# Kernel tuning notes

Measured on AMD Instinct MI355X. Metric: run time of the kernel, lower is better.

The kernel has to match this reference:

```python
import jax, jax.numpy as jnp
import numpy as np

A = 128       # atom_fea_len
NBR = 41      # nbr_fea_len
H = 128       # h_fea_len_dist == h_fea_len_const
NCONV = 3
EPS = 1e-5    # BatchNorm eps


def leaky(x):
    return jnp.where(x >= 0, x, 0.01 * x)  # LeakyReLU(0.01)


def bn(x2d, g, b):
    # training-mode BatchNorm1d: batch statistics over dim 0 (biased variance)
    mu = x2d.mean(0)
    var = x2d.var(0)
    return g * (x2d - mu) * jax.lax.rsqrt(var + EPS) + b


def setup_inputs() -> dict:
    N, M = 20000, 12
    key = jax.random.key(0)
    ks = jax.random.split(key, 24)
    s = 0.02
    in2 = 2 * A + NBR  # 297
    d = {}
    d["atom_fea"] = jax.random.normal(ks[0], (N, 92), jnp.float32)
    d["nbr_fea"] = jax.random.uniform(ks[1], (N, M, NBR), dtype=jnp.float32)
    d["nbr_fea_offset"] = jax.random.normal(ks[2], (N, M, 3), jnp.float32)
    d["atom_pos"] = jax.random.normal(ks[3], (N, 3), jnp.float32) * 3.0
    d["cells"] = jnp.eye(3, dtype=jnp.float32) * 10.0 + 0.1 * jax.random.normal(ks[4], (3, 3), jnp.float32)
    d["nbr_fea_idx"] = jax.random.randint(ks[5], (N, M), 0, N)
    # embedding
    d["emb_W"] = s * jax.random.normal(ks[6], (A, 92), jnp.float32)
    d["emb_b"] = jnp.zeros((A,), jnp.float32)
    # conv layers (stacked)
    d["convs_W"] = s * jax.random.normal(ks[7], (NCONV, 2 * A, in2), jnp.float32)
    d["convs_b"] = jnp.zeros((NCONV, 2 * A), jnp.float32)
    d["convs_bn1_g"] = jnp.ones((NCONV, 2 * A), jnp.float32)
    d["convs_bn1_b"] = jnp.zeros((NCONV, 2 * A), jnp.float32)
    d["convs_bn2_g"] = jnp.ones((NCONV, A), jnp.float32)
    d["convs_bn2_b"] = jnp.zeros((NCONV, A), jnp.float32)
    # bond_distance head
    d["dist_W"] = s * jax.random.normal(ks[8], (H, in2), jnp.float32)
    d["dist_b"] = jnp.zeros((H,), jnp.float32)
    d["dist_bn_g"] = jnp.ones((H,), jnp.float32)
    d["dist_bn_b"] = jnp.zeros((H,), jnp.float32)
    d["dist2_W"] = s * jax.random.normal(ks[9], (1, H), jnp.float32)
    d["dist2_b"] = jnp.zeros((1,), jnp.float32)
    # bond_constant head
    d["const_W"] = s * jax.random.normal(ks[10], (H, in2), jnp.float32)
    d["const_b"] = jnp.zeros((H,), jnp.float32)
    d["const_bn_g"] = jnp.ones((H,), jnp.float32)
    d["const_bn_b"] = jnp.zeros((H,), jnp.float32)
    d["const2_W"] = s * jax.random.normal(ks[11], (1, H), jnp.float32)
    d["const2_b"] = jnp.zeros((1,), jnp.float32)
    return d


def _forward(atom_fea, nbr_fea, nbr_fea_offset, atom_pos, cells,
             emb_W, emb_b, convs_W, convs_b, convs_bn1_g, convs_bn1_b,
             convs_bn2_g, convs_bn2_b, dist_W, dist_b, dist_bn_g, dist_bn_b,
             dist2_W, dist2_b, const_W, const_b, const_bn_g, const_bn_b,
             const2_W, const2_b, nbr_fea_idx):
    N, M = nbr_fea_idx.shape
    af = atom_fea @ emb_W.T + emb_b  # (N, A) embedding

    # get_distance: PBC distance using fractional offsets and the cell matrix
    nbr_abs = atom_pos[nbr_fea_idx] + jnp.einsum('nmk,kd->nmd', nbr_fea_offset, cells)
    dvec = nbr_abs - atom_pos[:, None, :]
    distance = jnp.sqrt(jnp.sum(dvec * dvec, -1, keepdims=True) + 1e-12)  # (N, M, 1)

    # conv layers: gather -> concat -> linear -> bn -> gate -> sum -> bn -> residual
    for i in range(NCONV):
        total = jnp.concatenate([
            jnp.broadcast_to(af[:, None, :], (N, M, A)),
            af[nbr_fea_idx],
            nbr_fea], axis=2)                                   # (N, M, 2A+NBR)
        g = jnp.einsum('nmf,of->nmo', total, convs_W[i]) + convs_b[i]  # (N, M, 2A)
        g = bn(g.reshape(-1, 2 * A), convs_bn1_g[i], convs_bn1_b[i]).reshape(N, M, 2 * A)
        nbr_filter = jax.nn.sigmoid(g[..., :A])
        nbr_core = leaky(g[..., A:])
        summed = bn((nbr_filter * nbr_core).sum(1), convs_bn2_g[i], convs_bn2_b[i])
        af = leaky(af + summed)

    # bond features
    bond_fea = jnp.concatenate([
        jnp.broadcast_to(af[:, None, :], (N, M, A)),
        af[nbr_fea_idx],
        nbr_fea], axis=2)  # (N, M, 2A+NBR)

    # bond_distance head (LeakyReLU activations)
    bd = jnp.einsum('nmf,hf->nmh', bond_fea, dist_W) + dist_b
    bd = leaky(bn(bd.reshape(-1, H), dist_bn_g, dist_bn_b).reshape(N, M, H))
    bd = leaky(jnp.einsum('nmh,oh->nmo', bd, dist2_W) + dist2_b + distance)  # (N, M, 1)

    # bond_constant head (Softplus activations)
    bc = jnp.einsum('nmf,hf->nmh', bond_fea, const_W) + const_b
    bc = jax.nn.softplus(bn(bc.reshape(-1, H), const_bn_g, const_bn_b).reshape(N, M, H))
    bc = jax.nn.softplus(jnp.einsum('nmh,oh->nmo', bc, const2_W) + const2_b)  # (N, M, 1)

    return jnp.concatenate([bd, bc], axis=-1)  # (N, M, 2)


def reference(atom_fea, nbr_fea, nbr_fea_offset, atom_pos, cells,
              emb_W, emb_b, convs_W, convs_b, convs_bn1_g, convs_bn1_b,
              convs_bn2_g, convs_bn2_b, dist_W, dist_b, dist_bn_g, dist_bn_b,
              dist2_W, dist2_b, const_W, const_b, const_bn_g, const_bn_b,
              const2_W, const2_b, nbr_fea_idx):
    return _forward(atom_fea, nbr_fea, nbr_fea_offset, atom_pos, cells,
                    emb_W, emb_b, convs_W, convs_b, convs_bn1_g, convs_bn1_b,
                    convs_bn2_g, convs_bn2_b, dist_W, dist_b, dist_bn_g, dist_bn_b,
                    dist2_W, dist2_b, const_W, const_b, const_bn_g, const_bn_b,
                    const2_W, const2_b, nbr_fea_idx)
```

## Files before the change

### kernel.cpp

```cpp
#include <hip/hip_runtime.h>
#include <hip/hip_bf16.h>
#include <math.h>

typedef __hip_bfloat16 bf16;

#define AFEA 128
#define NBRF 41
#define IN2 297
#define KP 320
#define TSTR 328
#define ROWS 64
#define P1 64
#define P2 16

typedef __attribute__((ext_vector_type(8))) short bf16x8;
typedef __attribute__((ext_vector_type(4))) float f32x4;

__device__ __forceinline__ unsigned short bfbits(float x) {
    bf16 h = __float2bfloat16(x);
    return *(unsigned short*)&h;
}
__device__ __forceinline__ unsigned int pack2(float x, float y) {
    return (unsigned int)bfbits(x) | ((unsigned int)bfbits(y) << 16);
}
__device__ __forceinline__ float blo(unsigned int u) { return __uint_as_float(u << 16); }
__device__ __forceinline__ float bhi(unsigned int u) { return __uint_as_float(u & 0xffff0000u); }
__device__ __forceinline__ float leakyf(float x) { return x >= 0.f ? x : 0.01f * x; }
__device__ __forceinline__ float sigmoid_fast(float x) { return 1.f / (1.f + __expf(-x)); }
__device__ __forceinline__ float softplus_fast(float x) {
    return fmaxf(x, 0.f) + __logf(1.f + __expf(-fabsf(x)));
}

__global__ void nbr16_kernel(const float* __restrict__ nbr, unsigned short* __restrict__ nbr16,
                             int NM)
{
    int i = blockIdx.x * blockDim.x + threadIdx.x;
    if (i >= NM * 64) return;
    int k = i & 63, e = i >> 6;
    nbr16[i] = (k < NBRF) ? bfbits(nbr[(size_t)e * NBRF + k]) : 0;
}

__global__ __launch_bounds__(256) void embed_kernel(
    const float* __restrict__ xf, const float* __restrict__ W,
    const float* __restrict__ b, float* __restrict__ af,
    unsigned short* __restrict__ af16, int N)
{
    __shared__ float W_s[92 * 128];
    __shared__ float xs[16 * 92];
    int t = threadIdx.x;
    int n0 = blockIdx.x * 16;
    for (int i = t; i < 92 * 128; i += 256) {
        int o = i / 92, k = i - o * 92;
        W_s[k * 128 + o] = W[i];
    }
    for (int i = t; i < 16 * 92; i += 256) {
        int a = i / 92, k = i - a * 92;
        int n = n0 + a;
        xs[i] = (n < N) ? xf[(size_t)n * 92 + k] : 0.f;
    }
    __syncthreads();
    int o = t & 127, h = t >> 7;
    float bias = b[o];
    for (int a = h; a < 16; a += 2) {
        int n = n0 + a;
        if (n >= N) break;
        float acc = bias;
        const float* xr = xs + a * 92;
        #pragma unroll 4
        for (int k = 0; k < 92; k++) acc += xr[k] * W_s[k * 128 + o];
        af[(size_t)n * AFEA + o] = acc;
        af16[(size_t)n * AFEA + o] = bfbits(acc);
    }
}

__global__ void prep_kernel(const float* __restrict__ Wa, size_t offA,
                            const float* __restrict__ Wsrc, size_t offB,
                            unsigned short* __restrict__ Wb,
                            float* __restrict__ zbuf, int nz)
{
    int i = blockIdx.x * blockDim.x + threadIdx.x;
    if (i < nz) zbuf[i] = 0.f;
    if (i >= KP * 256) return;
    int t32 = i & 31;
    int c = (i >> 5) & 255;
    int kc = i >> 13;
    int k = kc * 32 + t32;
    float v = 0.f;
    if (k < IN2) v = (c < 128) ? Wa[offA + (size_t)c * IN2 + k]
                               : Wsrc[offB + (size_t)(c - 128) * IN2 + k];
    Wb[i] = bfbits(v);
}

__global__ __launch_bounds__(256, 3) void gemm_mfma_kernel(
    const unsigned short* __restrict__ af16, const unsigned short* __restrict__ nbr16,
    const int* __restrict__ idx, const unsigned short* __restrict__ Wb,
    const float* __restrict__ bias_a, size_t boffA,
    const float* __restrict__ bias_b, size_t boffB,
    unsigned short* __restrict__ g_t, float* __restrict__ part1,
    int NM, int M)
{
    __shared__ unsigned short a_tile[ROWS * TSTR];
    const int t = threadIdx.x;
    const int e0 = blockIdx.x * ROWS;

    const int l = t & 63, w = t >> 6;
    const int m16 = l & 15, q = l >> 4;
    const int colbase = w * 64;
    const unsigned short* bbase = Wb + (size_t)(colbase + m16) * 32 + q * 8;

    {
        int row = t >> 2, p = t & 3;
        int e = e0 + row;
        int n = e / M;
        int j = idx[e];
        const uint4* srcn = (const uint4*)(af16 + (size_t)n * AFEA);
        const uint4* srcj = (const uint4*)(af16 + (size_t)j * AFEA);
        const uint4* srcb = (const uint4*)(nbr16 + (size_t)e * 64);
        uint4* dst = (uint4*)(a_tile + row * TSTR);
        #pragma unroll
        for (int u = 0; u < 4; u++) dst[p + 4 * u] = srcn[p + 4 * u];
        #pragma unroll
        for (int u = 0; u < 4; u++) dst[16 + p + 4 * u] = srcj[p + 4 * u];
        #pragma unroll
        for (int u = 0; u < 2; u++) dst[32 + p + 4 * u] = srcb[p + 4 * u];
    }

    bf16x8 bcur[4], bnxt[4];
    #pragma unroll
    for (int ct = 0; ct < 4; ct++)
        bcur[ct] = *(const bf16x8*)(bbase + ct * 512);
    #pragma unroll
    for (int ct = 0; ct < 4; ct++)
        bnxt[ct] = *(const bf16x8*)(bbase + 8192 + ct * 512);

    __syncthreads();

    f32x4 acc[4][4];
    #pragma unroll
    for (int rt = 0; rt < 4; rt++)
        #pragma unroll
        for (int ct = 0; ct < 4; ct++) acc[rt][ct] = (f32x4)0.f;

    const unsigned short* abase = a_tile + m16 * TSTR + q * 8;

    #pragma unroll
    for (int kc = 0; kc < KP / 32; kc++) {
        bf16x8 a[4], b2[4];
        if (kc < KP / 32 - 2) {
            #pragma unroll
            for (int ct = 0; ct < 4; ct++)
                b2[ct] = *(const bf16x8*)(bbase + (kc + 2) * 8192 + ct * 512);
        }
        #pragma unroll
        for (int rt = 0; rt < 4; rt++)
            a[rt] = *(const bf16x8*)(abase + rt * 16 * TSTR + kc * 32);
        #pragma unroll
        for (int rt = 0; rt < 4; rt++)
            #pragma unroll
            for (int ct = 0; ct < 4; ct++)
                acc[rt][ct] = __builtin_amdgcn_mfma_f32_16x16x32_bf16(
                    a[rt], bcur[ct], acc[rt][ct], 0, 0, 0);
        if (kc < KP / 32 - 1) {
            #pragma unroll
            for (int ct = 0; ct < 4; ct++) bcur[ct] = bnxt[ct];
        }
        if (kc < KP / 32 - 2) {
            #pragma unroll
            for (int ct = 0; ct < 4; ct++) bnxt[ct] = b2[ct];
        }
    }

    float* pp = part1 + (size_t)(blockIdx.x & (P1 - 1)) * 512;
    #pragma unroll
    for (int ct = 0; ct < 4; ct++) {
        int col = colbase + ct * 16 + m16;
        float bias = (col < 128) ? bias_a[boffA + col] : bias_b[boffB + col - 128];
        float ps = 0.f, pq = 0.f;
        #pragma unroll
        for (int rt = 0; rt < 4; rt++) {
            float v0 = acc[rt][ct][0] + bias;
            float v1 = acc[rt][ct][1] + bias;
            float v2 = acc[rt][ct][2] + bias;
            float v3 = acc[rt][ct][3] + bias;
            ps += (v0 + v1) + (v2 + v3);
            pq += (v0 * v0 + v1 * v1) + (v2 * v2 + v3 * v3);
            uint2 pk;
            pk.x = pack2(v0, v1);
            pk.y = pack2(v2, v3);
            *(uint2*)(g_t + (size_t)col * NM + e0 + rt * 16 + q * 4) = pk;
        }
        ps += __shfl_xor(ps, 16); ps += __shfl_xor(ps, 32);
        pq += __shfl_xor(pq, 16); pq += __shfl_xor(pq, 32);
        if (q == 0) {
            atomicAdd(&pp[col], ps);
            atomicAdd(&pp[256 + col], pq);
        }
    }
}

__global__ __launch_bounds__(256) void gate_kernel(
    const unsigned short* __restrict__ gt, const float* __restrict__ part1,
    const float* __restrict__ gamma, const float* __restrict__ beta,
    float* __restrict__ summed, float* __restrict__ part2,
    float cnt1, int N, int M, int NM)
{
    __shared__ float affA[4 * 16], affC[4 * 16];
    int t = threadIdx.x, w = t >> 6, l = t & 63;
    int cp0 = (blockIdx.x & 3) * 16 + w * 4;
    int fch0 = 2 * cp0;

    if (l < 16) {
        int ch = (l < 8) ? (fch0 + l) : (128 + fch0 + (l - 8));
        float s = 0.f, qq = 0.f;
        #pragma unroll 8
        for (int p = 0; p < P1; p++) {
            s += part1[(size_t)p * 512 + ch];
            qq += part1[(size_t)p * 512 + 256 + ch];
        }
        float mean = s / cnt1;
        float var = fmaxf(qq / cnt1 - mean * mean, 0.f);
        float a = gamma[ch] * rsqrtf(var + 1e-5f);
        affA[w * 16 + l] = a;
        affC[w * 16 + l] = beta[ch] - mean * a;
    }
    __syncthreads();

    int n = (blockIdx.x >> 2) * 64 + l;
    bool act = (n < N);
    size_t col0 = (size_t)n * M;
    float* pp = part2 + (size_t)(blockIdx.x & (P2 - 1)) * 256;
    #pragma unroll
    for (int cpi = 0; cpi < 4; cpi++) {
        int chf = fch0 + 2 * cpi;
        int chc = 128 + chf;
        float s0 = 0.f, s1 = 0.f;
        if (act) {
            const uint2* rf0 = (const uint2*)(gt + (size_t)chf * NM + col0);
            const uint2* rf1 = (const uint2*)(gt + (size_t)(chf + 1) * NM + col0);
            const uint2* rc0 = (const uint2*)(gt + (size_t)chc * NM + col0);
            const uint2* rc1 = (const uint2*)(gt + (size_t)(chc + 1) * NM + col0);
            float aF0 = affA[w * 16 + 2 * cpi],     cF0 = affC[w * 16 + 2 * cpi];
            float aF1 = affA[w * 16 + 2 * cpi + 1], cF1 = affC[w * 16 + 2 * cpi + 1];
            float aC0 = affA[w * 16 + 8 + 2 * cpi],     cC0 = affC[w * 16 + 8 + 2 * cpi];
            float aC1 = affA[w * 16 + 8 + 2 * cpi + 1], cC1 = affC[w * 16 + 8 + 2 * cpi + 1];
            #pragma unroll
            for (int u = 0; u < 3; u++) {
                uint2 f0 = rf0[u], f1 = rf1[u], k0 = rc0[u], k1 = rc1[u];
                #pragma unroll
                for (int h = 0; h < 4; h++) {
                    unsigned int fw0 = (h < 2) ? f0.x : f0.y;
                    unsigned int fw1 = (h < 2) ? f1.x : f1.y;
                    unsigned int kw0 = (h < 2) ? k0.x : k0.y;
                    unsigned int kw1 = (h < 2) ? k1.x : k1.y;
                    float gf0 = (h & 1) ? bhi(fw0) : blo(fw0);
                    float gf1 = (h & 1) ? bhi(fw1) : blo(fw1);
                    float gc0 = (h & 1) ? bhi(kw0) : blo(kw0);
                    float gc1 = (h & 1) ? bhi(kw1) : blo(kw1);
                    s0 += sigmoid_fast(fmaf(aF0, gf0, cF0)) * leakyf(fmaf(aC0, gc0, cC0));
                    s1 += sigmoid_fast(fmaf(aF1, gf1, cF1)) * leakyf(fmaf(aC1, gc1, cC1));
                }
            }
            *(float2*)(summed + (size_t)n * AFEA + chf) = make_float2(s0, s1);
        }
        float q0 = s0 * s0, q1 = s1 * s1;
        #pragma unroll
        for (int sft = 32; sft > 0; sft >>= 1) {
            s0 += __shfl_xor(s0, sft);
            s1 += __shfl_xor(s1, sft);
            q0 += __shfl_xor(q0, sft);
            q1 += __shfl_xor(q1, sft);
        }
        if (l == 0) {
            atomicAdd(&pp[chf], s0);
            atomicAdd(&pp[chf + 1], s1);
            atomicAdd(&pp[128 + chf], q0);
            atomicAdd(&pp[128 + chf + 1], q1);
        }
    }
}

__global__ __launch_bounds__(256) void afup_kernel(
    float* __restrict__ af, unsigned short* __restrict__ af16,
    const float* __restrict__ summed, const float* __restrict__ part2,
    const float* __restrict__ gamma2, const float* __restrict__ beta2,
    float cnt2, int total)
{
    __shared__ float a2s[128], c2s[128];
    int t = threadIdx.x;
    if (t < 128) {
        float s = 0.f, qq = 0.f;
        #pragma unroll
        for (int p = 0; p < P2; p++) {
            s += part2[(size_t)p * 256 + t];
            qq += part2[(size_t)p * 256 + 128 + t];
        }
        float mean = s / cnt2;
        float var = fmaxf(qq / cnt2 - mean * mean, 0.f);
        float a = gamma2[t] * rsqrtf(var + 1e-5f);
        a2s[t] = a;
        c2s[t] = beta2[t] - mean * a;
    }
    __syncthreads();
    int o = t & 127;
    float a2 = a2s[o], c2 = c2s[o];
    int base = blockIdx.x * 2048 + t;
    #pragma unroll
    for (int k = 0; k < 8; k++) {
        int i = base + k * 256;
        if (i < total) {
            float v = af[i] + a2 * summed[i] + c2;
            v = (v >= 0.f) ? v : 0.01f * v;
            af[i] = v;
            af16[i] = bfbits(v);
        }
    }
}

__global__ __launch_bounds__(256) void head_kernel(
    const unsigned short* __restrict__ gt, const float* __restrict__ part1,
    const float* __restrict__ dbg, const float* __restrict__ cbg,
    const float* __restrict__ dbb, const float* __restrict__ cbb,
    const float* __restrict__ w2d, const float* __restrict__ b2d,
    const float* __restrict__ w2c, const float* __restrict__ b2c,
    const float* __restrict__ pos, const float* __restrict__ off,
    const float* __restrict__ cells, const int* __restrict__ idx,
    float* __restrict__ out, float cnt1, int NM, int M)
{
    __shared__ float a_s[256], c_s[256], w_s[256];
    int t = threadIdx.x;
    {
        float s = 0.f, qq = 0.f;
        #pragma unroll 8
        for (int p = 0; p < P1; p++) {
            s += part1[(size_t)p * 512 + t];
            qq += part1[(size_t)p * 512 + 256 + t];
        }
        float mean = s / cnt1;
        float var = fmaxf(qq / cnt1 - mean * mean, 0.f);
        float g  = (t < 128) ? dbg[t] : cbg[t - 128];
        float be = (t < 128) ? dbb[t] : cbb[t - 128];
        float a = g * rsqrtf(var + 1e-5f);
        a_s[t] = a;
        c_s[t] = be - mean * a;
        w_s[t] = (t < 128) ? w2d[t] : w2c[t - 128];
    }
    __syncthreads();

    int e = blockIdx.x * 512 + t * 2;
    if (e >= NM) return;
    float sd0 = 0.f, sd1 = 0.f, sc0 = 0.f, sc1 = 0.f;
    #pragma unroll 4
    for (int ch = 0; ch < 128; ch++) {
        unsigned int u = *(const unsigned int*)(gt + (size_t)ch * NM + e);
        float a = a_s[ch], c = c_s[ch], wv = w_s[ch];
        sd0 += leakyf(fmaf(a, blo(u), c)) * wv;
        sd1 += leakyf(fmaf(a, bhi(u), c)) * wv;
    }
    #pragma unroll 4
    for (int ch = 128; ch < 256; ch++) {
        unsigned int u = *(const unsigned int*)(gt + (size_t)ch * NM + e);
        float a = a_s[ch], c = c_s[ch], wv = w_s[ch];
        sc0 += softplus_fast(fmaf(a, blo(u), c)) * wv;
        sc1 += softplus_fast(fmaf(a, bhi(u), c)) * wv;
    }
    float dist[2];
    #pragma unroll
    for (int h = 0; h < 2; h++) {
        int eb = e + h;
        int n = eb / M;
        int j = idx[eb];
        float o0 = off[(size_t)eb * 3 + 0];
        float o1 = off[(size_t)eb * 3 + 1];
        float o2 = off[(size_t)eb * 3 + 2];
        float d0 = o0 * cells[0] + o1 * cells[3] + o2 * cells[6] + pos[(size_t)j * 3 + 0] - pos[(size_t)n * 3 + 0];
        float d1 = o0 * cells[1] + o1 * cells[4] + o2 * cells[7] + pos[(size_t)j * 3 + 1] - pos[(size_t)n * 3 + 1];
        float d2 = o0 * cells[2] + o1 * cells[5] + o2 * cells[8] + pos[(size_t)j * 3 + 2] - pos[(size_t)n * 3 + 2];
        dist[h] = sqrtf(d0 * d0 + d1 * d1 + d2 * d2 + 1e-12f);
    }
    float bd = b2d[0], bc = b2c[0];
    float4 o4;
    o4.x = leakyf(sd0 + bd + dist[0]);
    o4.y = softplus_fast(sc0 + bc);
    o4.z = leakyf(sd1 + bd + dist[1]);
    o4.w = softplus_fast(sc1 + bc);
    *(float4*)(out + (size_t)e * 2) = o4;
}

extern "C" void kernel_launch(void* const* d_in, const int* in_sizes, int n_in,
                              void* d_out, int out_size, void* d_ws, size_t ws_size,
                              hipStream_t stream) {
    const float* atom_fea   = (const float*)d_in[0];
    const float* nbr_fea    = (const float*)d_in[1];
    const float* nbr_off    = (const float*)d_in[2];
    const float* atom_pos   = (const float*)d_in[3];
    const float* cells      = (const float*)d_in[4];
    const int*   idx        = (const int*)d_in[5];
    const float* emb_W      = (const float*)d_in[6];
    const float* emb_b      = (const float*)d_in[7];
    const float* convs_W    = (const float*)d_in[8];
    const float* convs_b    = (const float*)d_in[9];
    const float* bn1g       = (const float*)d_in[10];
    const float* bn1b       = (const float*)d_in[11];
    const float* bn2g       = (const float*)d_in[12];
    const float* bn2b       = (const float*)d_in[13];
    const float* dist_W     = (const float*)d_in[14];
    const float* dist_b     = (const float*)d_in[15];
    const float* dist_bn_g  = (const float*)d_in[16];
    const float* dist_bn_b  = (const float*)d_in[17];
    const float* dist2_W    = (const float*)d_in[18];
    const float* dist2_b    = (const float*)d_in[19];
    const float* const_W    = (const float*)d_in[20];
    const float* const_b    = (const float*)d_in[21];
    const float* const_bn_g = (const float*)d_in[22];
    const float* const_bn_b = (const float*)d_in[23];
    const float* const2_W   = (const float*)d_in[24];
    const float* const2_b   = (const float*)d_in[25];

    const int N  = in_sizes[0] / 92;
    const int M  = in_sizes[5] / N;
    const int NM = N * M;

    char* ws = (char*)d_ws;
    size_t off = 0;
    float* af             = (float*)(ws + off); off += (size_t)N * AFEA * 4;
    float* summed         = (float*)(ws + off); off += (size_t)N * AFEA * 4;
    unsigned short* af16  = (unsigned short*)(ws + off); off += (size_t)N * AFEA * 2;
    unsigned short* Wb    = (unsigned short*)(ws + off); off += (size_t)256 * KP * 2;
    float* part1          = (float*)(ws + off); off += (size_t)P1 * 512 * 4;
    float* part2          = (float*)(ws + off); off += (size_t)P2 * 256 * 4;
    unsigned short* g_t   = (unsigned short*)(ws + off); off += (size_t)NM * 256 * 2;
    unsigned short* nbr16 = (unsigned short*)(ws + off); off += (size_t)NM * 64 * 2;

    const int NPART = P1 * 512 + P2 * 256;

    nbr16_kernel<<<(NM * 64 + 255) / 256, 256, 0, stream>>>(nbr_fea, nbr16, NM);
    embed_kernel<<<(N + 15) / 16, 256, 0, stream>>>(atom_fea, emb_W, emb_b, af, af16, N);

    const int gblocks = NM / ROWS;
    const int gateblocks = ((N + 63) / 64) * 4;
    const int prepblocks = (256 * KP + 255) / 256;

    for (int i = 0; i < 3; i++) {
        size_t wo  = (size_t)i * 256 * IN2;
        size_t bo  = (size_t)i * 256;
        size_t b2o = (size_t)i * 128;

        prep_kernel<<<prepblocks, 256, 0, stream>>>(
            convs_W, wo, convs_W, wo + (size_t)128 * IN2, Wb, part1, NPART);
        gemm_mfma_kernel<<<gblocks, 256, 0, stream>>>(
            af16, nbr16, idx, Wb, convs_b, bo, convs_b, bo + 128,
            g_t, part1, NM, M);
        gate_kernel<<<gateblocks, 256, 0, stream>>>(
            g_t, part1, bn1g + bo, bn1b + bo, summed, part2, (float)NM, N, M, NM);
        afup_kernel<<<(N * AFEA + 2047) / 2048, 256, 0, stream>>>(
            af, af16, summed, part2, bn2g + b2o, bn2b + b2o, (float)N, N * AFEA);
    }

    {
        prep_kernel<<<prepblocks, 256, 0, stream>>>(
            dist_W, 0, const_W, 0, Wb, part1, P1 * 512);
        gemm_mfma_kernel<<<gblocks, 256, 0, stream>>>(
            af16, nbr16, idx, Wb, dist_b, 0, const_b, 0,
            g_t, part1, NM, M);
        head_kernel<<<(NM + 511) / 512, 256, 0, stream>>>(
            g_t, part1, dist_bn_g, const_bn_g, dist_bn_b, const_bn_b,
            dist2_W, dist2_b, const2_W, const2_b,
            atom_pos, nbr_off, cells, idx, (float*)d_out, (float)NM, NM, M);
    }
}
```

Before: 675.5 us.

## Hoist weight prep into one launch, fold stat zeroing, and rework gate kernel tiling

All four bf16 weight layouts are converted up front in a single prep kernel, which removes the per-layer prep launches. Zeroing of the partial-statistics buffers moves into the GEMM and afup kernels. The gate kernel is restructured so each thread handles two atoms with 16-byte loads over 16 channels, and results are staged in shared memory so the writes to summed are coalesced. The costs are a larger weight workspace and cross-kernel ordering assumptions for zeroing part1 and part2.

```diff
diff --git a/kernel.cpp b/kernel.cpp
--- a/kernel.cpp
+++ b/kernel.cpp
@@ -29,6 +29,13 @@
 __device__ __forceinline__ float sigmoid_fast(float x) { return 1.f / (1.f + __expf(-x)); }
 __device__ __forceinline__ float softplus_fast(float x) {
     return fmaxf(x, 0.f) + __logf(1.f + __expf(-fabsf(x)));
+}
+
+__device__ __forceinline__ float gpair(unsigned int fu, unsigned int cu,
+                                       float aF, float cF, float aC, float cC) {
+    float r = sigmoid_fast(fmaf(aF, blo(fu), cF)) * leakyf(fmaf(aC, blo(cu), cC));
+    r += sigmoid_fast(fmaf(aF, bhi(fu), cF)) * leakyf(fmaf(aC, bhi(cu), cC));
+    return r;
 }
 
 __global__ void nbr16_kernel(const float* __restrict__ nbr, unsigned short* __restrict__ nbr16,
@@ -73,40 +80,38 @@
     }
 }
 
-__global__ void prep_kernel(const float* __restrict__ Wa, size_t offA,
-                            const float* __restrict__ Wsrc, size_t offB,
-                            unsigned short* __restrict__ Wb,
-                            float* __restrict__ zbuf, int nz)
+__global__ void prep_all_kernel(const float* __restrict__ convs_W,
+                                const float* __restrict__ dist_W,
+                                const float* __restrict__ const_W,
+                                unsigned short* __restrict__ Wb4,
+                                float* __restrict__ zbuf, int nz)
 {
     int i = blockIdx.x * blockDim.x + threadIdx.x;
     if (i < nz) zbuf[i] = 0.f;
-    if (i >= KP * 256) return;
-    int t32 = i & 31;
-    int c = (i >> 5) & 255;
-    int kc = i >> 13;
+    if (i >= 4 * KP * 256) return;
+    int s = i / (KP * 256);
+    int r = i - s * (KP * 256);
+    int t32 = r & 31;
+    int c = (r >> 5) & 255;
+    int kc = r >> 13;
     int k = kc * 32 + t32;
     float v = 0.f;
-    if (k < IN2) v = (c < 128) ? Wa[offA + (size_t)c * IN2 + k]
-                               : Wsrc[offB + (size_t)(c - 128) * IN2 + k];
-    Wb[i] = bfbits(v);
-}
-
-__global__ __launch_bounds__(256, 3) void gemm_mfma_kernel(
+    if (k < IN2) {
+        if (s < 3) v = convs_W[((size_t)s * 256 + c) * IN2 + k];
+        else       v = (c < 128) ? dist_W[(size_t)c * IN2 + k]
+                                 : const_W[(size_t)(c - 128) * IN2 + k];
+    }
+    Wb4[i] = bfbits(v);
+}
+
+__device__ __forceinline__ void gemm_core(
     const unsigned short* __restrict__ af16, const unsigned short* __restrict__ nbr16,
     const int* __restrict__ idx, const unsigned short* __restrict__ Wb,
-    const float* __restrict__ bias_a, size_t boffA,
-    const float* __restrict__ bias_b, size_t boffB,
-    unsigned short* __restrict__ g_t, float* __restrict__ part1,
-    int NM, int M)
-{
-    __shared__ unsigned short a_tile[ROWS * TSTR];
-    const int t = threadIdx.x;
-    const int e0 = blockIdx.x * ROWS;
-
+    unsigned short* a_tile, int e0, int M, int t, f32x4 (&acc)[4][4])
+{
     const int l = t & 63, w = t >> 6;
     const int m16 = l & 15, q = l >> 4;
-    const int colbase = w * 64;
-    const unsigned short* bbase = Wb + (size_t)(colbase + m16) * 32 + q * 8;
+    const unsigned short* bbase = Wb + (size_t)(w * 64 + m16) * 32 + q * 8;
 
     {
         int row = t >> 2, p = t & 3;
@@ -135,7 +140,6 @@
 
     __syncthreads();
 
-    f32x4 acc[4][4];
     #pragma unroll
     for (int rt = 0; rt < 4; rt++)
         #pragma unroll
@@ -169,12 +173,30 @@
             for (int ct = 0; ct < 4; ct++) bnxt[ct] = b2[ct];
         }
     }
-
+}
+
+__global__ __launch_bounds__(256, 3) void gemm_mfma_kernel(
+    const unsigned short* __restrict__ af16, const unsigned short* __restrict__ nbr16,
+    const int* __restrict__ idx, const unsigned short* __restrict__ Wb,
+    const float* __restrict__ bias_a, const float* __restrict__ bias_b,
+    unsigned short* __restrict__ g_t, float* __restrict__ part1,
+    float* __restrict__ part2, int NM, int M)
+{
+    __shared__ __align__(16) unsigned short a_tile[ROWS * TSTR];
+    int t = threadIdx.x;
+    const int e0 = blockIdx.x * ROWS;
+
+    if (blockIdx.x < 16) part2[blockIdx.x * 256 + t] = 0.f;
+
+    f32x4 acc[4][4];
+    gemm_core(af16, nbr16, idx, Wb, a_tile, e0, M, t, acc);
+
+    const int l = t & 63, w = t >> 6, m16 = l & 15, q = l >> 4;
     float* pp = part1 + (size_t)(blockIdx.x & (P1 - 1)) * 512;
     #pragma unroll
     for (int ct = 0; ct < 4; ct++) {
-        int col = colbase + ct * 16 + m16;
-        float bias = (col < 128) ? bias_a[boffA + col] : bias_b[boffB + col - 128];
+        int col = w * 64 + ct * 16 + m16;
+        float bias = (col < 128) ? bias_a[col] : bias_b[col - 128];
         float ps = 0.f, pq = 0.f;
         #pragma unroll
         for (int rt = 0; rt < 4; rt++) {
@@ -202,15 +224,15 @@
     const unsigned short* __restrict__ gt, const float* __restrict__ part1,
     const float* __restrict__ gamma, const float* __restrict__ beta,
     float* __restrict__ summed, float* __restrict__ part2,
-    float cnt1, int N, int M, int NM)
-{
-    __shared__ float affA[4 * 16], affC[4 * 16];
+    float cnt1, int N, int NM)
+{
+    __shared__ float affA[32], affC[32];
+    __shared__ float ls[128 * 17];
     int t = threadIdx.x, w = t >> 6, l = t & 63;
-    int cp0 = (blockIdx.x & 3) * 16 + w * 4;
-    int fch0 = 2 * cp0;
-
-    if (l < 16) {
-        int ch = (l < 8) ? (fch0 + l) : (128 + fch0 + (l - 8));
+    int ab = blockIdx.x >> 3, pg = blockIdx.x & 7;
+
+    if (t < 32) {
+        int ch = (t < 16) ? (pg * 16 + t) : (128 + pg * 16 + (t - 16));
         float s = 0.f, qq = 0.f;
         #pragma unroll 8
         for (int p = 0; p < P1; p++) {
@@ -220,62 +242,55 @@
         float mean = s / cnt1;
         float var = fmaxf(qq / cnt1 - mean * mean, 0.f);
         float a = gamma[ch] * rsqrtf(var + 1e-5f);
-        affA[w * 16 + l] = a;
-        affC[w * 16 + l] = beta[ch] - mean * a;
-    }
-    __syncthreads();
-
-    int n = (blockIdx.x >> 2) * 64 + l;
-    bool act = (n < N);
-    size_t col0 = (size_t)n * M;
+        affA[t] = a;
+        affC[t] = beta[ch] - mean * a;
+    }
+    __syncthreads();
+
+    int n0 = ab * 128 + 2 * l;
+    bool a0 = n0 < N, a1 = (n0 + 1) < N;
     float* pp = part2 + (size_t)(blockIdx.x & (P2 - 1)) * 256;
-    #pragma unroll
-    for (int cpi = 0; cpi < 4; cpi++) {
-        int chf = fch0 + 2 * cpi;
-        int chc = 128 + chf;
+
+    #pragma unroll
+    for (int pi = 0; pi < 4; pi++) {
+        int plocal = w * 4 + pi;
+        int chf = pg * 16 + plocal;
+        float aF = affA[plocal],      cF = affC[plocal];
+        float aC = affA[16 + plocal], cC = affC[16 + plocal];
         float s0 = 0.f, s1 = 0.f;
-        if (act) {
-            const uint2* rf0 = (const uint2*)(gt + (size_t)chf * NM + col0);
-            const uint2* rf1 = (const uint2*)(gt + (size_t)(chf + 1) * NM + col0);
-            const uint2* rc0 = (const uint2*)(gt + (size_t)chc * NM + col0);
-            const uint2* rc1 = (const uint2*)(gt + (size_t)(chc + 1) * NM + col0);
-            float aF0 = affA[w * 16 + 2 * cpi],     cF0 = affC[w * 16 + 2 * cpi];
-            float aF1 = affA[w * 16 + 2 * cpi + 1], cF1 = affC[w * 16 + 2 * cpi + 1];
-            float aC0 = affA[w * 16 + 8 + 2 * cpi],     cC0 = affC[w * 16 + 8 + 2 * cpi];
-            float aC1 = affA[w * 16 + 8 + 2 * cpi + 1], cC1 = affC[w * 16 + 8 + 2 * cpi + 1];
-            #pragma unroll
-            for (int u = 0; u < 3; u++) {
-                uint2 f0 = rf0[u], f1 = rf1[u], k0 = rc0[u], k1 = rc1[u];
-                #pragma unroll
-                for (int h = 0; h < 4; h++) {
-                    unsigned int fw0 = (h < 2) ? f0.x : f0.y;
-                    unsigned int fw1 = (h < 2) ? f1.x : f1.y;
-                    unsigned int kw0 = (h < 2) ? k0.x : k0.y;
-                    unsigned int kw1 = (h < 2) ? k1.x : k1.y;
-                    float gf0 = (h & 1) ? bhi(fw0) : blo(fw0);
-                    float gf1 = (h & 1) ? bhi(fw1) : blo(fw1);
-                    float gc0 = (h & 1) ? bhi(kw0) : blo(kw0);
-                    float gc1 = (h & 1) ? bhi(kw1) : blo(kw1);
-                    s0 += sigmoid_fast(fmaf(aF0, gf0, cF0)) * leakyf(fmaf(aC0, gc0, cC0));
-                    s1 += sigmoid_fast(fmaf(aF1, gf1, cF1)) * leakyf(fmaf(aC1, gc1, cC1));
-                }
-            }
-            *(float2*)(summed + (size_t)n * AFEA + chf) = make_float2(s0, s1);
-        }
-        float q0 = s0 * s0, q1 = s1 * s1;
+        if (a0) {
+            const uint4* F = (const uint4*)(gt + (size_t)chf * NM + (size_t)n0 * 12);
+            const uint4* C = (const uint4*)(gt + (size_t)(chf + 128) * NM + (size_t)n0 * 12);
+            uint4 f0 = F[0], f1 = F[1], f2 = F[2];
+            uint4 c0 = C[0], c1 = C[1], c2 = C[2];
+            s0 = gpair(f0.x, c0.x, aF, cF, aC, cC) + gpair(f0.y, c0.y, aF, cF, aC, cC)
+               + gpair(f0.z, c0.z, aF, cF, aC, cC) + gpair(f0.w, c0.w, aF, cF, aC, cC)
+               + gpair(f1.x, c1.x, aF, cF, aC, cC) + gpair(f1.y, c1.y, aF, cF, aC, cC);
+            s1 = gpair(f1.z, c1.z, aF, cF, aC, cC) + gpair(f1.w, c1.w, aF, cF, aC, cC)
+               + gpair(f2.x, c2.x, aF, cF, aC, cC) + gpair(f2.y, c2.y, aF, cF, aC, cC)
+               + gpair(f2.z, c2.z, aF, cF, aC, cC) + gpair(f2.w, c2.w, aF, cF, aC, cC);
+            if (!a1) s1 = 0.f;
+            ls[(2 * l) * 17 + plocal] = s0;
+            if (a1) ls[(2 * l + 1) * 17 + plocal] = s1;
+        }
+        float sr = s0 + s1;
+        float qr = s0 * s0 + s1 * s1;
         #pragma unroll
         for (int sft = 32; sft > 0; sft >>= 1) {
-            s0 += __shfl_xor(s0, sft);
-            s1 += __shfl_xor(s1, sft);
-            q0 += __shfl_xor(q0, sft);
-            q1 += __shfl_xor(q1, sft);
+            sr += __shfl_xor(sr, sft);
+            qr += __shfl_xor(qr, sft);
         }
         if (l == 0) {
-            atomicAdd(&pp[chf], s0);
-            atomicAdd(&pp[chf + 1], s1);
-            atomicAdd(&pp[128 + chf], q0);
-            atomicAdd(&pp[128 + chf + 1], q1);
-        }
+            atomicAdd(&pp[chf], sr);
+            atomicAdd(&pp[128 + chf], qr);
+        }
+    }
+    __syncthreads();
+
+    for (int i = t; i < 128 * 16; i += 256) {
+        int a = i >> 4, c = i & 15;
+        int n = ab * 128 + a;
+        if (n < N) summed[(size_t)n * AFEA + pg * 16 + c] = ls[a * 17 + c];
     }
 }
 
@@ -283,10 +298,11 @@
     float* __restrict__ af, unsigned short* __restrict__ af16,
     const float* __restrict__ summed, const float* __restrict__ part2,
     const float* __restrict__ gamma2, const float* __restrict__ beta2,
-    float cnt2, int total)
+    float* __restrict__ part1, float cnt2, int total)
 {
     __shared__ float a2s[128], c2s[128];
     int t = threadIdx.x;
+    if (blockIdx.x < 128) part1[blockIdx.x * 256 + t] = 0.f;
     if (t < 128) {
         float s = 0.f, qq = 0.f;
         #pragma unroll
@@ -425,7 +441,7 @@
     float* af             = (float*)(ws + off); off += (size_t)N * AFEA * 4;
     float* summed         = (float*)(ws + off); off += (size_t)N * AFEA * 4;
     unsigned short* af16  = (unsigned short*)(ws + off); off += (size_t)N * AFEA * 2;
-    unsigned short* Wb    = (unsigned short*)(ws + off); off += (size_t)256 * KP * 2;
+    unsigned short* Wb4   = (unsigned short*)(ws + off); off += (size_t)4 * 256 * KP * 2;
     float* part1          = (float*)(ws + off); off += (size_t)P1 * 512 * 4;
     float* part2          = (float*)(ws + off); off += (size_t)P2 * 256 * 4;
     unsigned short* g_t   = (unsigned short*)(ws + off); off += (size_t)NM * 256 * 2;
@@ -433,35 +449,31 @@
 
     const int NPART = P1 * 512 + P2 * 256;
 
+    prep_all_kernel<<<(4 * KP * 256 + 255) / 256, 256, 0, stream>>>(
+        convs_W, dist_W, const_W, Wb4, part1, NPART);
     nbr16_kernel<<<(NM * 64 + 255) / 256, 256, 0, stream>>>(nbr_fea, nbr16, NM);
     embed_kernel<<<(N + 15) / 16, 256, 0, stream>>>(atom_fea, emb_W, emb_b, af, af16, N);
 
     const int gblocks = NM / ROWS;
-    const int gateblocks = ((N + 63) / 64) * 4;
-    const int prepblocks = (256 * KP + 255) / 256;
+    const int gateblocks = ((N + 127) / 128) * 8;
 
     for (int i = 0; i < 3; i++) {
-        size_t wo  = (size_t)i * 256 * IN2;
-        size_t bo  = (size_t)i * 256;
-        size_t b2o = (size_t)i * 128;
-
-        prep_kernel<<<prepblocks, 256, 0, stream>>>(
-            convs_W, wo, convs_W, wo + (size_t)128 * IN2, Wb, part1, NPART);
+        const unsigned short* Wbi = Wb4 + (size_t)i * KP * 256;
+        const float* cb = convs_b + (size_t)i * 256;
         gemm_mfma_kernel<<<gblocks, 256, 0, stream>>>(
-            af16, nbr16, idx, Wb, convs_b, bo, convs_b, bo + 128,
-            g_t, part1, NM, M);
+            af16, nbr16, idx, Wbi, cb, cb + 128, g_t, part1, part2, NM, M);
         gate_kernel<<<gateblocks, 256, 0, stream>>>(
-            g_t, part1, bn1g + bo, bn1b + bo, summed, part2, (float)NM, N, M, NM);
+            g_t, part1, bn1g + (size_t)i * 256, bn1b + (size_t)i * 256,
+            summed, part2, (float)NM, N, NM);
         afup_kernel<<<(N * AFEA + 2047) / 2048, 256, 0, stream>>>(
-            af, af16, summed, part2, bn2g + b2o, bn2b + b2o, (float)N, N * AFEA);
+            af, af16, summed, part2, bn2g + (size_t)i * 128, bn2b + (size_t)i * 128,
+            part1, (float)N, N * AFEA);
     }
 
     {
-        prep_kernel<<<prepblocks, 256, 0, stream>>>(
-            dist_W, 0, const_W, 0, Wb, part1, P1 * 512);
         gemm_mfma_kernel<<<gblocks, 256, 0, stream>>>(
-            af16, nbr16, idx, Wb, dist_b, 0, const_b, 0,
-            g_t, part1, NM, M);
+            af16, nbr16, idx, Wb4 + (size_t)3 * KP * 256, dist_b, const_b,
+            g_t, part1, part2, NM, M);
         head_kernel<<<(NM + 511) / 512, 256, 0, stream>>>(
             g_t, part1, dist_bn_g, const_bn_g, dist_bn_b, const_bn_b,
             dist2_W, dist2_b, const2_W, const2_b,
```

Measured after the change: 665.5 us. No clear change (-1.5%).
